# Kernel tuning notes

Measured on AMD Instinct MI355X. Metric: run time of the kernel, lower is better.

## Reference

```python
import jax, jax.numpy as jnp
import numpy as np

NUM_ITERS = 3
EPS = 1e-8


def squash(t, axis=-1):
    sq = jnp.sum(t * t, axis=axis, keepdims=True)
    scale = sq / (1.0 + sq)
    return scale * t / jnp.sqrt(sq + EPS)


def setup_inputs() -> dict:
    key = jax.random.key(0)
    k1, k2 = jax.random.split(key)
    B, Nin, Din, Nout, Dout = 32, 2048, 16, 64, 32
    x = jax.random.normal(k1, (B, Nin, Din), dtype=jnp.float32)
    W = jax.random.normal(k2, (1, Nin, Nout, Dout, Din), dtype=jnp.float32)
    return {"x": x, "W": W}


def reference(x, W):
    # x: [B, Nin, Din]; W: [1, Nin, Nout, Dout, Din]
    # u_hat[b,n,o,d] = sum_i W[0,n,o,d,i] * x[b,n,i]
    u_hat = jnp.einsum('nodi,bni->bnod', W[0], x)  # [B, Nin, Nout, Dout]
    B, Nin, Nout, _ = u_hat.shape
    b = jnp.zeros((B, Nin, Nout, 1), dtype=u_hat.dtype)
    v = None
    for it in range(NUM_ITERS):
        c = jax.nn.softmax(b, axis=2)              # [B, Nin, Nout, 1]
        s = jnp.sum(c * u_hat, axis=1)             # [B, Nout, Dout]
        v = squash(s, axis=-1)                     # [B, Nout, Dout]
        if it < NUM_ITERS - 1:
            agreement = jnp.sum(u_hat * v[:, None], axis=-1, keepdims=True)
            b = b + agreement
    return v
```

## Files before the change

### kernel.cpp

```cpp
#include <hip/hip_runtime.h>


#define B_   32
#define NIN  2048
#define DIN  16
#define NOUT 64
#define DOUT 32
#define BQ   8
#define NCHB 16
#define CG   (NIN / NCHB)
#define NBLK (CG * (B_ / BQ))
#define TPB  1024
#define PART_PER_BLK (BQ * NOUT * DOUT / 2)
#define NC2   64
#define NCHK  (NIN / NC2)
#define NBLK2 (B_ * NCHK)
#define TPB2  512

__device__ __forceinline__ unsigned pack_bf16(float a, float b) {
    unsigned ia = __float_as_uint(a), ib = __float_as_uint(b);
    ia += 0x7fffu + ((ia >> 16) & 1u);
    ib += 0x7fffu + ((ib >> 16) & 1u);
    return (ia >> 16) | (ib & 0xffff0000u);
}

__global__ __launch_bounds__(TPB)
void caps_pass1u(const float* __restrict__ W, const float* __restrict__ x,
                 unsigned* __restrict__ uws, float2* __restrict__ part)
{
    const int t  = threadIdx.x;
    const int o  = t >> 4;
    const int dg = t & 15;
    const int d0 = dg << 1;

    const int bid  = blockIdx.x;
    const int xcd  = bid & 7;
    const int j    = bid >> 3;
    const int cg   = xcd * (CG / 8) + (j >> 2);
    const int quad = j & 3;
    const int nbase = cg * NCHB;
    const int bbase = quad * BQ;

    __shared__ float4 xs[BQ][NCHB * DIN / 4];

    if (t < BQ * NCHB * DIN / 4) {
        const int bb = t >> 6;
        const int k  = t & 63;
        xs[bb][k] = ((const float4*)x)[(size_t)(bbase + bb) * (NIN * DIN / 4)
                                       + (size_t)nbase * (DIN / 4) + k];
    }

    float acc0[BQ], acc1[BQ];
#pragma unroll
    for (int bb = 0; bb < BQ; ++bb) { acc0[bb] = 0.f; acc1[bb] = 0.f; }

    __syncthreads();

    for (int nn = 0; nn < NCHB; ++nn) {
        const int n = nbase + nn;
        const float4* wp = (const float4*)(W +
            (((size_t)n * NOUT + o) * DOUT + d0) * DIN);
        float4 w[8];
#pragma unroll
        for (int q = 0; q < 8; ++q) w[q] = wp[q];
#pragma unroll
        for (int bb = 0; bb < BQ; ++bb) {
            const float4* xr = &xs[bb][nn * 4];
            float u0 = 0.f, u1 = 0.f;
#pragma unroll
            for (int q = 0; q < 4; ++q) {
                const float4 xv = xr[q];
                u0 += w[q].x*xv.x + w[q].y*xv.y + w[q].z*xv.z + w[q].w*xv.w;
                u1 += w[4+q].x*xv.x + w[4+q].y*xv.y + w[4+q].z*xv.z + w[4+q].w*xv.w;
            }
            acc0[bb] += u0;
            acc1[bb] += u1;
            uws[((size_t)(bbase + bb) * NIN + n) * 1024 + t] = pack_bf16(u0, u1);
        }
    }

#pragma unroll
    for (int bb = 0; bb < BQ; ++bb) {
        float2* base = part + (size_t)(cg * 4 + quad) * PART_PER_BLK;
        base[bb * (NOUT * DOUT / 2) + o * (DOUT / 2) + dg] =
            make_float2(acc0[bb] * (1.0f / 64.0f), acc1[bb] * (1.0f / 64.0f));
    }
}

__global__ __launch_bounds__(TPB2)
void caps_pass23u(const unsigned* __restrict__ uws, const float* __restrict__ v_in,
                  float* __restrict__ part2)
{
    const int t    = threadIdx.x;
    const int o    = t >> 3;
    const int dg   = t & 7;
    const int d0   = dg << 2;
    const int lane = t & 63;

    const int bid   = blockIdx.x;
    const int b     = bid >> 5;
    const int chunk = bid & 31;
    const int nbase = chunk * NC2;

    __shared__ float lg[2][NOUT];

    const float4 vv = *(const float4*)(v_in + ((size_t)b * NOUT + o) * DOUT + d0);

    float a0 = 0.f, a1 = 0.f, a2 = 0.f, a3 = 0.f;

    const uint2* ub = (const uint2*)uws + ((size_t)b * NIN + nbase) * 512 + t;

    for (int nn = 0; nn < NC2; ++nn) {
        const uint2 up = ub[(size_t)nn * 512];
        const float u0 = __uint_as_float(up.x << 16);
        const float u1 = __uint_as_float(up.x & 0xffff0000u);
        const float u2 = __uint_as_float(up.y << 16);
        const float u3 = __uint_as_float(up.y & 0xffff0000u);

        float p = u0*vv.x + u1*vv.y + u2*vv.z + u3*vv.w;
        p += __shfl_xor(p, 1);
        p += __shfl_xor(p, 2);
        p += __shfl_xor(p, 4);
        const int par = nn & 1;
        if (dg == 0) lg[par][o] = p;
        __syncthreads();

        const float e = __expf(lg[par][lane]);
        float sm = e;
#pragma unroll
        for (int m = 1; m < 64; m <<= 1) sm += __shfl_xor(sm, m);
        const float c = __shfl(e, o) / sm;

        a0 += c * u0; a1 += c * u1; a2 += c * u2; a3 += c * u3;
    }

    *(float4*)(part2 + ((size_t)(b * NCHK + chunk) * (NOUT * DOUT)) + o * DOUT + d0)
        = make_float4(a0, a1, a2, a3);
}

__global__ __launch_bounds__(256)
void reduce_squash2(const float* __restrict__ part2, float* __restrict__ vout,
                    int accumulate)
{
    const int id = blockIdx.x * 256 + threadIdx.x;
    const float* p = part2 + (size_t)(id >> 11) * (NCHK * NOUT * DOUT) + (id & 2047);
    float s = 0.f;
#pragma unroll 8
    for (int ch = 0; ch < NCHK; ++ch) s += p[(size_t)ch * (NOUT * DOUT)];

    float sq = s * s;
#pragma unroll
    for (int m = 1; m < 32; m <<= 1) sq += __shfl_xor(sq, m);
    const float f = sq / ((1.0f + sq) * sqrtf(sq + 1e-8f));
    const float v = s * f;
    if (accumulate) vout[id] += v;
    else            vout[id] = v;
}

template<int PASS, bool ATOMIC>
__global__ __launch_bounds__(TPB)
void caps_pass(const float* __restrict__ W, const float* __restrict__ x,
               const float* __restrict__ v_in, float* __restrict__ s_out,
               float2* __restrict__ part)
{
    const int t    = threadIdx.x;
    const int o    = t >> 4;
    const int dg   = t & 15;
    const int d0   = dg << 1;
    const int lane = t & 63;
    const int wid  = t >> 6;

    const int bid  = blockIdx.x;
    const int xcd  = bid & 7;
    const int j    = bid >> 3;
    const int cg   = xcd * (CG / 8) + (j >> 2);
    const int quad = j & 3;
    const int nbase = cg * NCHB;
    const int bbase = quad * BQ;

    __shared__ float4 xs[BQ][NCHB * DIN / 4];

    if (t < BQ * NCHB * DIN / 4) {
        const int bb = t >> 6;
        const int k  = t & 63;
        xs[bb][k] = ((const float4*)x)[(size_t)(bbase + bb) * (NIN * DIN / 4)
                                       + (size_t)nbase * (DIN / 4) + k];
    }

    float acc0[BQ], acc1[BQ];
#pragma unroll
    for (int bb = 0; bb < BQ; ++bb) { acc0[bb] = 0.f; acc1[bb] = 0.f; }

    __syncthreads();

    if constexpr (PASS == 1) {
        for (int nn = 0; nn < NCHB; ++nn) {
            const float4* wp = (const float4*)(W +
                (((size_t)(nbase + nn) * NOUT + o) * DOUT + d0) * DIN);
            float4 w[8];
#pragma unroll
            for (int q = 0; q < 8; ++q) w[q] = wp[q];
#pragma unroll
            for (int bb = 0; bb < BQ; ++bb) {
                const float4* xr = &xs[bb][nn * 4];
                float u0 = 0.f, u1 = 0.f;
#pragma unroll
                for (int q = 0; q < 4; ++q) {
                    const float4 xv = xr[q];
                    u0 += w[q].x*xv.x + w[q].y*xv.y + w[q].z*xv.z + w[q].w*xv.w;
                    u1 += w[4+q].x*xv.x + w[4+q].y*xv.y + w[4+q].z*xv.z + w[4+q].w*xv.w;
                }
                acc0[bb] += u0;
                acc1[bb] += u1;
            }
        }
    } else {
        __shared__ float  lg[BQ * NOUT];
        __shared__ float  cs[BQ * NOUT];
        __shared__ float2 ustash[BQ][TPB];
        for (int nn = 0; nn < NCHB; ++nn) {
            const float4* wp = (const float4*)(W +
                (((size_t)(nbase + nn) * NOUT + o) * DOUT + d0) * DIN);
            float4 w[8];
#pragma unroll
            for (int q = 0; q < 8; ++q) w[q] = wp[q];
#pragma unroll
            for (int bb = 0; bb < BQ; ++bb) {
                const float4* xr = &xs[bb][nn * 4];
                float u0 = 0.f, u1 = 0.f;
#pragma unroll
                for (int q = 0; q < 4; ++q) {
                    const float4 xv = xr[q];
                    u0 += w[q].x*xv.x + w[q].y*xv.y + w[q].z*xv.z + w[q].w*xv.w;
                    u1 += w[4+q].x*xv.x + w[4+q].y*xv.y + w[4+q].z*xv.z + w[4+q].w*xv.w;
                }
                const float2 vvv = ((const float2*)v_in)[
                    (size_t)(bbase + bb) * (NOUT * DOUT / 2) + o * (DOUT / 2) + dg];
                float p = u0 * vvv.x + u1 * vvv.y;
                p += __shfl_xor(p, 1);
                p += __shfl_xor(p, 2);
                p += __shfl_xor(p, 4);
                p += __shfl_xor(p, 8);
                if (dg == 0) lg[bb * NOUT + o] = p;
                ustash[bb][t] = make_float2(u0, u1);
            }
            __syncthreads();
            if (wid < BQ) {
                const float e = __expf(lg[wid * NOUT + lane]);
                float sm = e;
#pragma unroll
                for (int m = 1; m < 64; m <<= 1) sm += __shfl_xor(sm, m);
                cs[wid * NOUT + lane] = e / sm;
            }
            __syncthreads();
#pragma unroll
            for (int bb = 0; bb < BQ; ++bb) {
                const float c = cs[bb * NOUT + o];
                const float2 u = ustash[bb][t];
                acc0[bb] += c * u.x;
                acc1[bb] += c * u.y;
            }
        }
    }

    const float scale = (PASS == 1) ? (1.0f / 64.0f) : 1.0f;
    if constexpr (ATOMIC) {
#pragma unroll
        for (int bb = 0; bb < BQ; ++bb) {
            float* dst = &s_out[((size_t)(bbase + bb) * NOUT + o) * DOUT + d0];
            atomicAdd(dst,     acc0[bb] * scale);
            atomicAdd(dst + 1, acc1[bb] * scale);
        }
    } else {
        float2* base = part + (size_t)(cg * 4 + quad) * PART_PER_BLK;
#pragma unroll
        for (int bb = 0; bb < BQ; ++bb)
            base[bb * (NOUT * DOUT / 2) + o * (DOUT / 2) + dg] =
                make_float2(acc0[bb] * scale, acc1[bb] * scale);
    }
}

__global__ __launch_bounds__(256)
void reduce_squash(const float2* __restrict__ part, float* __restrict__ vout,
                   int accumulate)
{
    const int id = blockIdx.x * 256 + threadIdx.x;
    const int dg = id & 15;
    const int o  = (id >> 4) & 63;
    const int b  = id >> 10;
    const int quad = b >> 3, bb = b & 7;
    const size_t base = (size_t)bb * (NOUT * DOUT / 2) + o * (DOUT / 2) + dg;

    float2 acc0 = make_float2(0.f, 0.f), acc1 = make_float2(0.f, 0.f);
    for (int cg = 0; cg < CG; cg += 2) {
        const float2 p0 = part[(size_t)(cg * 4 + quad) * PART_PER_BLK + base];
        const float2 p1 = part[(size_t)((cg + 1) * 4 + quad) * PART_PER_BLK + base];
        acc0.x += p0.x; acc0.y += p0.y;
        acc1.x += p1.x; acc1.y += p1.y;
    }
    const float sx = acc0.x + acc1.x, sy = acc0.y + acc1.y;

    float sq = sx * sx + sy * sy;
    sq += __shfl_xor(sq, 1);
    sq += __shfl_xor(sq, 2);
    sq += __shfl_xor(sq, 4);
    sq += __shfl_xor(sq, 8);
    const float f = sq / ((1.0f + sq) * sqrtf(sq + 1e-8f));

    float2* vo = (float2*)vout;
    float2 r = make_float2(sx * f, sy * f);
    if (accumulate) {
        const float2 old = vo[id];
        r.x += old.x; r.y += old.y;
    }
    vo[id] = r;
}

__global__ void squash_k(const float* __restrict__ s, float* __restrict__ vout,
                         int accumulate)
{
    const int idx = blockIdx.x * 256 + threadIdx.x;
    const float val = s[idx];
    float sq = val * val;
#pragma unroll
    for (int m = 1; m < 32; m <<= 1) sq += __shfl_xor(sq, m);
    const float f = sq / ((1.0f + sq) * sqrtf(sq + 1e-8f));
    const float v = val * f;
    if (accumulate) vout[idx] += v;
    else            vout[idx] = v;
}

extern "C" void kernel_launch(void* const* d_in, const int* in_sizes, int n_in,
                              void* d_out, int out_size, void* d_ws, size_t ws_size,
                              hipStream_t stream)
{
    (void)in_sizes; (void)n_in; (void)out_size;
    const float* x = (const float*)d_in[0];
    const float* W = (const float*)d_in[1];
    float* out = (float*)d_out;

    const size_t uBytes    = (size_t)B_ * NIN * NOUT * DOUT * 2;
    const size_t partBytes = (size_t)NBLK * PART_PER_BLK * sizeof(float2);
    const size_t vBytes    = (size_t)B_ * NOUT * DOUT * sizeof(float);

    if (ws_size >= uBytes + partBytes + vBytes) {
        unsigned* uws  = (unsigned*)d_ws;
        float2*   p1   = (float2*)((char*)d_ws + uBytes);
        float*    p2   = (float*)p1;
        float*    vA   = (float*)((char*)d_ws + uBytes + partBytes);

        caps_pass1u<<<dim3(NBLK), dim3(TPB), 0, stream>>>(W, x, uws, p1);
        reduce_squash<<<dim3(128), dim3(256), 0, stream>>>(p1, vA, 0);

        caps_pass23u<<<dim3(NBLK2), dim3(TPB2), 0, stream>>>(uws, vA, p2);
        reduce_squash2<<<dim3(256), dim3(256), 0, stream>>>(p2, vA, 1);

        caps_pass23u<<<dim3(NBLK2), dim3(TPB2), 0, stream>>>(uws, vA, p2);
        reduce_squash2<<<dim3(256), dim3(256), 0, stream>>>(p2, out, 0);
    } else if (ws_size >= partBytes + vBytes) {
        float2* part = (float2*)d_ws;
        float*  vA   = (float*)((char*)d_ws + partBytes);

        caps_pass<1, false><<<dim3(NBLK), dim3(TPB), 0, stream>>>(W, x, nullptr, nullptr, part);
        reduce_squash<<<dim3(128), dim3(256), 0, stream>>>(part, vA, 0);

        caps_pass<2, false><<<dim3(NBLK), dim3(TPB), 0, stream>>>(W, x, vA, nullptr, part);
        reduce_squash<<<dim3(128), dim3(256), 0, stream>>>(part, vA, 1);

        caps_pass<2, false><<<dim3(NBLK), dim3(TPB), 0, stream>>>(W, x, vA, nullptr, part);
        reduce_squash<<<dim3(128), dim3(256), 0, stream>>>(part, out, 0);
    } else {
        float* s  = (float*)d_ws;
        float* vA = s + B_ * NOUT * DOUT;

        hipMemsetAsync(s, 0, vBytes, stream);
        caps_pass<1, true><<<dim3(NBLK), dim3(TPB), 0, stream>>>(W, x, nullptr, s, nullptr);
        squash_k<<<dim3(256), dim3(256), 0, stream>>>(s, vA, 0);

        hipMemsetAsync(s, 0, vBytes, stream);
        caps_pass<2, true><<<dim3(NBLK), dim3(TPB), 0, stream>>>(W, x, vA, s, nullptr);
        squash_k<<<dim3(256), dim3(256), 0, stream>>>(s, vA, 1);

        hipMemsetAsync(s, 0, vBytes, stream);
        caps_pass<2, true><<<dim3(NBLK), dim3(TPB), 0, stream>>>(W, x, vA, s, nullptr);
        squash_k<<<dim3(256), dim3(256), 0, stream>>>(s, out, 0);
    }
}
```

Before: 372.9 us.

## Transpose u_hat workspace layout so each lane owns one output capsule

Pass 1 now stores the packed bf16 u_hat workspace with the output-capsule index fastest, as [b][n][dg][o]. In pass 2/3 each thread owns one capsule and holds all 32 Dout values in registers, so the logit dot product is computed per thread. The softmax now needs only a single wavefront shuffle reduction, which removes the shared-memory exchange and the __syncthreads on every input capsule. Each block now covers 8 batches with 16-row chunks, giving more partial chunks for the final reduction and higher register pressure per thread.

```diff
diff --git a/kernel.cpp b/kernel.cpp
--- a/kernel.cpp
+++ b/kernel.cpp
@@ -12,9 +12,9 @@
 #define NBLK (CG * (B_ / BQ))
 #define TPB  1024
 #define PART_PER_BLK (BQ * NOUT * DOUT / 2)
-#define NC2   64
-#define NCHK  (NIN / NC2)
-#define NBLK2 (B_ * NCHK)
+#define NC2   16
+#define NCHK2 (NIN / NC2)
+#define NBLK2 ((B_ / 8) * NCHK2)
 #define TPB2  512
 
 __device__ __forceinline__ unsigned pack_bf16(float a, float b) {
@@ -29,8 +29,8 @@
                  unsigned* __restrict__ uws, float2* __restrict__ part)
 {
     const int t  = threadIdx.x;
-    const int o  = t >> 4;
-    const int dg = t & 15;
+    const int o  = t & 63;
+    const int dg = t >> 6;
     const int d0 = dg << 1;
 
     const int bid  = blockIdx.x;
@@ -63,6 +63,7 @@
         float4 w[8];
 #pragma unroll
         for (int q = 0; q < 8; ++q) w[q] = wp[q];
+        unsigned* urow = uws + (((size_t)bbase * NIN + n) * 16 + dg) * 64 + o;
 #pragma unroll
         for (int bb = 0; bb < BQ; ++bb) {
             const float4* xr = &xs[bb][nn * 4];
@@ -75,7 +76,7 @@
             }
             acc0[bb] += u0;
             acc1[bb] += u1;
-            uws[((size_t)(bbase + bb) * NIN + n) * 1024 + t] = pack_bf16(u0, u1);
+            urow[(size_t)bb * (NIN * 1024)] = pack_bf16(u0, u1);
         }
     }
 
@@ -92,50 +93,62 @@
                   float* __restrict__ part2)
 {
     const int t    = threadIdx.x;
-    const int o    = t >> 3;
-    const int dg   = t & 7;
-    const int d0   = dg << 2;
-    const int lane = t & 63;
+    const int o    = t & 63;
+    const int wid  = t >> 6;
 
     const int bid   = blockIdx.x;
-    const int b     = bid >> 5;
-    const int chunk = bid & 31;
+    const int b     = (bid >> 7) * 8 + wid;
+    const int chunk = bid & 127;
     const int nbase = chunk * NC2;
 
-    __shared__ float lg[2][NOUT];
-
-    const float4 vv = *(const float4*)(v_in + ((size_t)b * NOUT + o) * DOUT + d0);
-
-    float a0 = 0.f, a1 = 0.f, a2 = 0.f, a3 = 0.f;
-
-    const uint2* ub = (const uint2*)uws + ((size_t)b * NIN + nbase) * 512 + t;
-
+    float vr[DOUT];
+    {
+        const float4* vp = (const float4*)(v_in + ((size_t)b * NOUT + o) * DOUT);
+#pragma unroll
+        for (int q = 0; q < 8; ++q) {
+            const float4 vv = vp[q];
+            vr[q*4+0] = vv.x; vr[q*4+1] = vv.y; vr[q*4+2] = vv.z; vr[q*4+3] = vv.w;
+        }
+    }
+
+    float acc[DOUT];
+#pragma unroll
+    for (int d = 0; d < DOUT; ++d) acc[d] = 0.f;
+
+    const unsigned* ub = uws + (((size_t)b * NIN + nbase) * 16) * 64 + o;
+
+#pragma unroll 1
     for (int nn = 0; nn < NC2; ++nn) {
-        const uint2 up = ub[(size_t)nn * 512];
-        const float u0 = __uint_as_float(up.x << 16);
-        const float u1 = __uint_as_float(up.x & 0xffff0000u);
-        const float u2 = __uint_as_float(up.y << 16);
-        const float u3 = __uint_as_float(up.y & 0xffff0000u);
-
-        float p = u0*vv.x + u1*vv.y + u2*vv.z + u3*vv.w;
-        p += __shfl_xor(p, 1);
-        p += __shfl_xor(p, 2);
-        p += __shfl_xor(p, 4);
-        const int par = nn & 1;
-        if (dg == 0) lg[par][o] = p;
-        __syncthreads();
-
-        const float e = __expf(lg[par][lane]);
+        const unsigned* un = ub + (size_t)nn * 1024;
+        unsigned up[16];
+#pragma unroll
+        for (int dg = 0; dg < 16; ++dg) up[dg] = un[dg * 64];
+
+        float logit = 0.f;
+#pragma unroll
+        for (int dg = 0; dg < 16; ++dg) {
+            const float uE = __uint_as_float(up[dg] << 16);
+            const float uO = __uint_as_float(up[dg] & 0xffff0000u);
+            logit += uE * vr[2*dg] + uO * vr[2*dg+1];
+        }
+        const float e = __expf(logit);
         float sm = e;
 #pragma unroll
         for (int m = 1; m < 64; m <<= 1) sm += __shfl_xor(sm, m);
-        const float c = __shfl(e, o) / sm;
-
-        a0 += c * u0; a1 += c * u1; a2 += c * u2; a3 += c * u3;
-    }
-
-    *(float4*)(part2 + ((size_t)(b * NCHK + chunk) * (NOUT * DOUT)) + o * DOUT + d0)
-        = make_float4(a0, a1, a2, a3);
+        const float c = e / sm;
+#pragma unroll
+        for (int dg = 0; dg < 16; ++dg) {
+            const float uE = __uint_as_float(up[dg] << 16);
+            const float uO = __uint_as_float(up[dg] & 0xffff0000u);
+            acc[2*dg]   += c * uE;
+            acc[2*dg+1] += c * uO;
+        }
+    }
+
+    float* pb = part2 + (((size_t)b * NCHK2 + chunk) * NOUT + o) * DOUT;
+#pragma unroll
+    for (int d = 0; d < DOUT; d += 4)
+        *(float4*)(pb + d) = make_float4(acc[d], acc[d+1], acc[d+2], acc[d+3]);
 }
 
 __global__ __launch_bounds__(256)
@@ -143,10 +156,10 @@
                     int accumulate)
 {
     const int id = blockIdx.x * 256 + threadIdx.x;
-    const float* p = part2 + (size_t)(id >> 11) * (NCHK * NOUT * DOUT) + (id & 2047);
+    const float* p = part2 + (size_t)(id >> 11) * (NCHK2 * NOUT * DOUT) + (id & 2047);
     float s = 0.f;
 #pragma unroll 8
-    for (int ch = 0; ch < NCHK; ++ch) s += p[(size_t)ch * (NOUT * DOUT)];
+    for (int ch = 0; ch < NCHK2; ++ch) s += p[(size_t)ch * (NOUT * DOUT)];
 
     float sq = s * s;
 #pragma unroll
@@ -291,14 +304,14 @@
     const int quad = b >> 3, bb = b & 7;
     const size_t base = (size_t)bb * (NOUT * DOUT / 2) + o * (DOUT / 2) + dg;
 
-    float2 acc0 = make_float2(0.f, 0.f), acc1 = make_float2(0.f, 0.f);
+    float2 a0 = make_float2(0.f, 0.f), a1 = make_float2(0.f, 0.f);
     for (int cg = 0; cg < CG; cg += 2) {
         const float2 p0 = part[(size_t)(cg * 4 + quad) * PART_PER_BLK + base];
         const float2 p1 = part[(size_t)((cg + 1) * 4 + quad) * PART_PER_BLK + base];
-        acc0.x += p0.x; acc0.y += p0.y;
-        acc1.x += p1.x; acc1.y += p1.y;
-    }
-    const float sx = acc0.x + acc1.x, sy = acc0.y + acc1.y;
+        a0.x += p0.x; a0.y += p0.y;
+        a1.x += p1.x; a1.y += p1.y;
+    }
+    const float sx = a0.x + a1.x, sy = a0.y + a1.y;
 
     float sq = sx * sx + sy * sy;
     sq += __shfl_xor(sq, 1);
```

After: 374.9 us. Within noise of the previous version (+0.5%).
